# Kernel tuning notes

Measured on AMD Instinct MI355X. Metric: run time of the kernel, lower is better.

## Reference

```python
import jax, jax.numpy as jnp
import numpy as np
import math

N = 50000          # nodes
E = 1000000        # edges (avg degree 20)
NGRAPH = 64        # graphs in batch
CIN = 16           # input scalar channels (16x0e)
C = 32             # hidden multiplicity (mul)
OUT = 100          # output scalars per graph (100x0e)
NB = 10            # number_of_basis
MAX_RADIUS = 3.5
NUM_NEIGH = 20.0
NUM_NODES = 781.25 # 50000 / 64


def setup_inputs() -> dict:
    key = jax.random.key(0)
    ks = jax.random.split(key, 24)
    def p(k, shape, fan):
        return jax.random.normal(k, shape, jnp.float32) / math.sqrt(fan)
    inp = {}
    inp['pos'] = jax.random.normal(ks[0], (N, 3), jnp.float32)
    inp['x'] = jax.random.normal(ks[1], (N, CIN), jnp.float32)
    inp['z'] = jnp.ones((N, 1), jnp.float32)
    inp['edge_index'] = jax.random.randint(ks[2], (2, E), 0, N)
    inp['edge_shift'] = jnp.zeros((E, 3), jnp.float32)
    inp['lattice'] = jax.random.normal(ks[3], (NGRAPH, 3, 3), jnp.float32) * 0.01
    inp['batch'] = jnp.sort(jax.random.randint(ks[4], (N,), 0, NGRAPH))
    inp['fc1_w0'] = p(ks[5], (NB, 100), NB)
    inp['fc1_w1'] = p(ks[6], (100, 2 * CIN), 100)
    inp['sc1'] = p(ks[7], (CIN, 2 * C), CIN)
    inp['lin1_s'] = p(ks[8], (CIN, 2 * C), CIN)
    inp['lin1_v'] = p(ks[9], (CIN, C), CIN)
    inp['fc2_w0'] = p(ks[10], (NB, 100), NB)
    inp['fc2_w1'] = p(ks[11], (100, 5 * C), 100)
    inp['sc2_s'] = p(ks[12], (C, 2 * C), C)
    inp['sc2_v'] = p(ks[13], (C, C), C)
    inp['lin2_s'] = p(ks[14], (C, 2 * C), C)
    inp['lin2_v'] = p(ks[15], (C, C), C)
    inp['fco_w0'] = p(ks[16], (NB, 100), NB)
    inp['fco_w1'] = p(ks[17], (100, 2 * C), 100)
    inp['sco'] = p(ks[18], (C, OUT), C)
    inp['lino_s'] = p(ks[19], (C, OUT), C)
    return inp


def _edge_features(pos, edge_index, edge_shift, lattice, batch):
    src, dst = edge_index[0], edge_index[1]
    ebatch = batch[src]
    # preprocess: edge vectors with periodic shift correction
    edge_vec = pos[dst] - pos[src] + jnp.einsum('ni,nij->nj', edge_shift, lattice[ebatch])
    r = jnp.linalg.norm(edge_vec, axis=1)
    rhat = edge_vec / jnp.maximum(r, 1e-12)[:, None]
    # spherical harmonics lmax=1, component normalization: Y0 = 1, Y1 = sqrt(3) * rhat
    sh0 = jnp.ones_like(r)
    sh1 = math.sqrt(3.0) * rhat
    # soft_one_hot_linspace, basis='gaussian', cutoff=False, scaled by sqrt(NB)
    values = jnp.linspace(0.0, MAX_RADIUS, NB)
    step = values[1] - values[0]
    diff = (r[:, None] - values[None, :]) / step
    basis = jnp.exp(-diff * diff) / 1.12 * math.sqrt(NB)
    # smooth_cutoff(r / max_radius)
    u = 2.0 * (r / MAX_RADIUS - 1.0)
    cut = jnp.where(u > 0, 0.0, jnp.where(u < -2.0, 1.0, 0.5 * (1.0 - jnp.cos(math.pi * u))))
    return src, dst, cut * sh0, cut[:, None] * sh1, basis


def _seg(m, dst):
    return jax.ops.segment_sum(m, dst, num_segments=N) / math.sqrt(NUM_NEIGH)


def reference(pos, x, z, edge_index, edge_shift, lattice, batch,
              fc1_w0, fc1_w1, sc1, lin1_s, lin1_v,
              fc2_w0, fc2_w1, sc2_s, sc2_v, lin2_s, lin2_v,
              fco_w0, fco_w1, sco, lino_s):
    src, dst, sh0, sh1, basis = _edge_features(pos, edge_index, edge_shift, lattice, batch)

    # ---- layer 1: 16x0e input -> gated (C x 0e, C x 1o) ----
    w = jax.nn.silu(basis @ fc1_w0) @ fc1_w1           # (E, 2*CIN) radial weights
    s_src = x[src]                                     # (E, CIN)
    m_s = w[:, :CIN] * s_src * sh0[:, None]            # 0e x Y0 -> 0e
    m_v = (w[:, CIN:] * s_src)[:, :, None] * sh1[:, None, :]  # 0e x Y1 -> 1o
    a_s = _seg(m_s, dst)                               # (N, CIN)
    a_v = _seg(m_v, dst)                               # (N, CIN, 3)
    s_h = (x * z) @ sc1 + a_s @ lin1_s                 # (N, 2C) scalars+gates
    v_h = jnp.einsum('nci,co->noi', a_v, lin1_v)       # (N, C, 3)
    s = jax.nn.silu(s_h[:, :C])
    v = v_h * jax.nn.sigmoid(s_h[:, C:])[:, :, None]

    # ---- layer 2: (C x 0e, C x 1o) -> gated (C x 0e, C x 1o) ----
    w = jax.nn.silu(basis @ fc2_w0) @ fc2_w1           # (E, 5C)
    w1, w2, w3, w4, w5 = jnp.split(w, 5, axis=1)
    ss = s[src]                                        # (E, C)
    vs = v[src]                                        # (E, C, 3)
    m_s = w1 * ss * sh0[:, None] + w2 * jnp.einsum('eci,ei->ec', vs, sh1)
    m_v = (w3 * ss)[:, :, None] * sh1[:, None, :] \
        + w4[:, :, None] * vs * sh0[:, None, None] \
        + w5[:, :, None] * jnp.cross(vs, sh1[:, None, :])
    a_s = _seg(m_s, dst)
    a_v = _seg(m_v, dst)
    s_h = (s * z) @ sc2_s + a_s @ lin2_s
    v_h = jnp.einsum('nci,co->noi', v, sc2_v) + jnp.einsum('nci,co->noi', a_v, lin2_v)
    s2 = jax.nn.silu(s_h[:, :C])
    v2 = v_h * jax.nn.sigmoid(s_h[:, C:])[:, :, None]

    # ---- output convolution: -> 100x0e per node ----
    w = jax.nn.silu(basis @ fco_w0) @ fco_w1           # (E, 2C)
    w1, w2 = jnp.split(w, 2, axis=1)
    m = w1 * s2[src] * sh0[:, None] + w2 * jnp.einsum('eci,ei->ec', v2[src], sh1)
    a = _seg(m, dst)                                   # (N, C)
    out_nodes = (s2 * z) @ sco + a @ lino_s            # (N, OUT)

    # reduce_output: scatter over graphs, divide sqrt(num_nodes)
    out = jax.ops.segment_sum(out_nodes, batch, num_segments=NGRAPH) / math.sqrt(NUM_NODES)
    return out
```

## Files before the change

kernel.cpp:

```cpp
#include <hip/hip_runtime.h>
#include <hip/hip_bf16.h>

#define NN 50000
#define EE 1000000
#define NGRAPHS 64
#define NB_N 196
#define NB_E 3907
#define NB_X 3125
#define NTAB 4096
#define SPL 16

#define INV_SQRT_NEIGH 0.22360679774997896f
#define INV_SQRT_NODES 0.035777087639996634f
#define SQRT3 1.7320508075688772f
#define BSCALE 2.8234621879136734f
#define BSTEP 0.3888888888888889f
#define INV_BSTEP 2.5714285714285716f
#define PI_F 3.14159265358979323846f
#define TAB_DR (3.5f / 4095.0f)
#define TAB_SCALE (4095.0f / 3.5f)

__device__ __forceinline__ float silu_f(float x) { return x / (1.0f + __expf(-x)); }
__device__ __forceinline__ float sigm_f(float x) { return 1.0f / (1.0f + __expf(-x)); }

__device__ __forceinline__ unsigned short f2bf(float f) {
    union { float f; unsigned u; } v; v.f = f;
    unsigned r = v.u + 0x7fffu + ((v.u >> 16) & 1u);
    return (unsigned short)(r >> 16);
}
__device__ __forceinline__ unsigned pk2(float a, float b) {
    return (unsigned)f2bf(a) | ((unsigned)f2bf(b) << 16);
}
__device__ __forceinline__ float bflo(unsigned u) { return __uint_as_float(u << 16); }
__device__ __forceinline__ float bfhi(unsigned u) { return __uint_as_float(u & 0xffff0000u); }

__global__ __launch_bounds__(256) void k_tab(
    const float* __restrict__ fc1w0, const float* __restrict__ fc1w1,
    const float* __restrict__ fc2w0, const float* __restrict__ fc2w1,
    const float* __restrict__ fcow0, const float* __restrict__ fcow1,
    float* __restrict__ tab1, unsigned short* __restrict__ tab2b,
    unsigned short* __restrict__ tab3b)
{
    __shared__ float h[3][100];
    int entry = blockIdx.x;
    int t = threadIdx.x;
    float r = entry * TAB_DR;
    float b[10];
#pragma unroll
    for (int i = 0; i < 10; ++i) {
        float d = (r - (float)i * BSTEP) * INV_BSTEP;
        b[i] = __expf(-d * d) * BSCALE;
    }
    for (int job = t; job < 300; job += 256) {
        int tb = job / 100;
        int j = job - tb * 100;
        const float* w0 = (tb == 0) ? fc1w0 : (tb == 1 ? fc2w0 : fcow0);
        float a = 0.0f;
#pragma unroll
        for (int i = 0; i < 10; ++i) a += b[i] * w0[i * 100 + j];
        h[tb][j] = silu_f(a);
    }
    __syncthreads();
    if (t < 32) {
        float acc = 0.0f;
        for (int j = 0; j < 100; ++j) acc += h[0][j] * fc1w1[j * 32 + t];
        tab1[(size_t)entry * 32 + t] = acc;
    } else if (t < 192) {
        int o = t - 32;
        float acc = 0.0f;
        for (int j = 0; j < 100; ++j) acc += h[1][j] * fc2w1[j * 160 + o];
        tab2b[((size_t)entry * 32 + (o & 31)) * 8 + (o >> 5)] = f2bf(acc);
    } else {
        int o = t - 192;
        float acc = 0.0f;
        for (int j = 0; j < 100; ++j) acc += h[2][j] * fcow1[j * 64 + o];
        tab3b[((size_t)entry * 32 + (o & 31)) * 2 + (o >> 5)] = f2bf(acc);
    }
}

__global__ __launch_bounds__(256) void k_pre2(
    const int* __restrict__ batch, int* __restrict__ gstart,
    const int* __restrict__ ei, int* __restrict__ deg,
    const float* __restrict__ x, unsigned short* __restrict__ row0)
{
    int blk = blockIdx.x;
    if (blk < NB_N) {
        int n = blk * 256 + threadIdx.x;
        if (n >= NN) return;
        int b = batch[n];
        if (n == 0) { for (int g = 0; g <= b; ++g) gstart[g] = 0; }
        else {
            int pb = batch[n - 1];
            for (int g = pb + 1; g <= b; ++g) gstart[g] = n;
        }
        if (n == NN - 1) { for (int g = b + 1; g <= NGRAPHS; ++g) gstart[g] = NN; }
    } else if (blk < NB_N + NB_E) {
        int e = (blk - NB_N) * 256 + threadIdx.x;
        if (e < EE) atomicAdd(&deg[ei[EE + e]], 1);
    } else {
        int idx = (blk - NB_N - NB_E) * 256 + threadIdx.x;
        if (idx < NN * 16) row0[idx] = f2bf(x[idx]);
    }
}

__global__ __launch_bounds__(256) void k_scan1(const int* __restrict__ deg, int* __restrict__ bsum)
{
    __shared__ int sd[256];
    int t = threadIdx.x;
    int i = blockIdx.x * 256 + t;
    sd[t] = (i < NN) ? deg[i] : 0;
    __syncthreads();
#pragma unroll
    for (int o = 128; o > 0; o >>= 1) {
        if (t < o) sd[t] += sd[t + o];
        __syncthreads();
    }
    if (t == 0) bsum[blockIdx.x] = sd[0];
}

__global__ void k_scan2(const int* __restrict__ bsum, int* __restrict__ boff, int* __restrict__ rowp)
{
    if (threadIdx.x == 0) {
        int acc = 0;
        for (int b = 0; b < NB_N; ++b) { boff[b] = acc; acc += bsum[b]; }
        rowp[NN] = EE;
    }
}

__global__ __launch_bounds__(256) void k_scan3(
    const int* __restrict__ deg, const int* __restrict__ boff,
    int* __restrict__ rowp, int* __restrict__ cursor)
{
    __shared__ int sd[256];
    int t = threadIdx.x;
    int i = blockIdx.x * 256 + t;
    int v = (i < NN) ? deg[i] : 0;
    sd[t] = v;
    __syncthreads();
#pragma unroll
    for (int o = 1; o < 256; o <<= 1) {
        int xv = 0;
        if (t >= o) xv = sd[t - o];
        __syncthreads();
        sd[t] += xv;
        __syncthreads();
    }
    if (i < NN) {
        int val = boff[blockIdx.x] + sd[t] - v;
        rowp[i] = val;
        cursor[i] = val;
    }
}

__global__ __launch_bounds__(256) void k_geom(
    const float* __restrict__ pos, const int* __restrict__ ei,
    const float* __restrict__ eshift, const float* __restrict__ lat,
    const int* __restrict__ batch, int* __restrict__ cursor,
    uint4* __restrict__ rec)
{
    int e = blockIdx.x * 256 + threadIdx.x;
    if (e >= EE) return;
    int src = ei[e];
    int dst = ei[EE + e];
    int g = batch[src];
    const float* L = lat + g * 9;
    float t0 = eshift[e*3+0], t1 = eshift[e*3+1], t2 = eshift[e*3+2];
    float vx = pos[dst*3+0] - pos[src*3+0] + t0*L[0] + t1*L[3] + t2*L[6];
    float vy = pos[dst*3+1] - pos[src*3+1] + t0*L[1] + t1*L[4] + t2*L[7];
    float vz = pos[dst*3+2] - pos[src*3+2] + t0*L[2] + t1*L[5] + t2*L[8];
    float r = sqrtf(vx*vx + vy*vy + vz*vz);
    float u = 2.0f * (r * (1.0f/3.5f) - 1.0f);
    float cut;
    if (u > 0.0f) cut = 0.0f;
    else if (u < -2.0f) cut = 1.0f;
    else cut = 0.5f * (1.0f - __cosf(PI_F * u));
    float inv = 1.0f / fmaxf(r, 1e-12f);
    float sc = SQRT3 * cut * inv;
    int i0 = (int)fminf(r * TAB_SCALE + 0.5f, 4095.0f);
    int slot = atomicAdd(&cursor[dst], 1);
    rec[slot] = make_uint4(pk2(sc * vx, sc * vy), pk2(sc * vz, 0.0f),
                           (unsigned)src | ((unsigned)i0 << 17),
                           __float_as_uint(cut));
}

#define EREC_DECODE(E)                                  \
    float cs_ = __uint_as_float((E).w);                 \
    float cx_ = bflo((E).x);                            \
    float cy_ = bfhi((E).x);                            \
    float cz_ = bflo((E).y);                            \
    int src_ = (int)((E).z & 0x1ffffu);                 \
    int i0_ = (int)((E).z >> 17);

#define F1_EDGE(E, ACC) {                                           \
    EREC_DECODE(E)                                                  \
    float w_ = tab1[(size_t)i0_ * 32 + toff];                       \
    float xs_ = __uint_as_float((unsigned)row0[src_ * 16 + c] << 16); \
    float gs_ = (q == 0) ? cs_ : (q == 1 ? cx_ : (q == 2 ? cy_ : cz_)); \
    ACC += w_ * xs_ * gs_; }

__global__ __launch_bounds__(256) void k_fuse1(
    const int* __restrict__ rowp, const uint4* __restrict__ rec,
    const float* __restrict__ tab1, const unsigned short* __restrict__ row0,
    float* __restrict__ a1)
{
    int wid = (blockIdx.x * 256 + threadIdx.x) >> 6;
    int l = threadIdx.x & 63;
    if (wid >= NN) return;
    int b0 = __builtin_amdgcn_readfirstlane(rowp[wid]);
    int b1 = __builtin_amdgcn_readfirstlane(rowp[wid + 1]);
    int q = l >> 4, c = l & 15;
    int toff = (q ? 16 : 0) + c;
    float aA = 0.0f, aB = 0.0f, aC = 0.0f, aD = 0.0f;
    int s = b0;
    for (; s + 3 < b1; s += 4) {
        uint4 eA = rec[s], eB = rec[s+1], eC = rec[s+2], eD = rec[s+3];
        F1_EDGE(eA, aA) F1_EDGE(eB, aB) F1_EDGE(eC, aC) F1_EDGE(eD, aD)
    }
    for (; s < b1; ++s) {
        uint4 eA = rec[s];
        F1_EDGE(eA, aA)
    }
    a1[(size_t)wid * 64 + l] = (aA + aB) + (aC + aD);
}

#define F2_EDGE(E, AS, AX, AY, AZ) {                                \
    EREC_DECODE(E)                                                  \
    uint4 tv_ = ((const uint4*)tab2b)[(size_t)i0_ * 32 + c];        \
    uint2 rv_ = ((const uint2*)row1)[(size_t)src_ * 32 + c];        \
    float w1_ = bflo(tv_.x), w2_ = bfhi(tv_.x);                     \
    float w3_ = bflo(tv_.y), w4_ = bfhi(tv_.y);                     \
    float w5_ = bflo(tv_.z);                                        \
    float sv_ = bflo(rv_.x), vx_ = bfhi(rv_.x);                     \
    float vy_ = bflo(rv_.y), vz_ = bfhi(rv_.y);                     \
    float dot_ = vx_ * cx_ + vy_ * cy_ + vz_ * cz_;                 \
    float w3s_ = w3_ * sv_, w4c_ = w4_ * cs_;                       \
    AS += w1_ * sv_ * cs_ + w2_ * dot_;                             \
    AX += w3s_ * cx_ + w4c_ * vx_ + w5_ * (vy_ * cz_ - vz_ * cy_);  \
    AY += w3s_ * cy_ + w4c_ * vy_ + w5_ * (vz_ * cx_ - vx_ * cz_);  \
    AZ += w3s_ * cz_ + w4c_ * vz_ + w5_ * (vx_ * cy_ - vy_ * cx_); }

__global__ __launch_bounds__(256) void k_fuse2(
    const int* __restrict__ rowp, const uint4* __restrict__ rec,
    const unsigned short* __restrict__ tab2b, const unsigned short* __restrict__ row1,
    float* __restrict__ a2)
{
    int wid = (blockIdx.x * 256 + threadIdx.x) >> 6;
    int l = threadIdx.x & 63;
    if (wid >= NN) return;
    int b0 = __builtin_amdgcn_readfirstlane(rowp[wid]);
    int b1 = __builtin_amdgcn_readfirstlane(rowp[wid + 1]);
    int p = l >> 5, c = l & 31;
    float s0 = 0, x0 = 0, y0 = 0, z0 = 0;
    float s1a = 0, x1 = 0, y1 = 0, z1 = 0;
    int s = b0 + p;
    for (; s + 4 < b1; s += 6) {
        uint4 eA = rec[s], eB = rec[s+2], eC = rec[s+4];
        F2_EDGE(eA, s0, x0, y0, z0)
        F2_EDGE(eB, s1a, x1, y1, z1)
        F2_EDGE(eC, s0, x0, y0, z0)
    }
    for (; s < b1; s += 2) {
        uint4 eA = rec[s];
        F2_EDGE(eA, s1a, x1, y1, z1)
    }
    float mS = s0 + s1a, mX = x0 + x1, mY = y0 + y1, mZ = z0 + z1;
    mS += __shfl_xor(mS, 32);
    mX += __shfl_xor(mX, 32);
    mY += __shfl_xor(mY, 32);
    mZ += __shfl_xor(mZ, 32);
    if (p == 0) {
        float* ap = a2 + (size_t)wid * 128;
        ap[c]      = mS;
        ap[32 + c] = mX;
        ap[64 + c] = mY;
        ap[96 + c] = mZ;
    }
}

#define F3_EDGE(E, ACC) {                                           \
    EREC_DECODE(E)                                                  \
    unsigned tv_ = ((const unsigned*)tab3b)[(size_t)i0_ * 32 + c];  \
    uint2 rv_ = ((const uint2*)row2)[(size_t)src_ * 32 + c];        \
    float w1_ = bflo(tv_), w2_ = bfhi(tv_);                         \
    float sv_ = bflo(rv_.x), vx_ = bfhi(rv_.x);                     \
    float vy_ = bflo(rv_.y), vz_ = bfhi(rv_.y);                     \
    float dot_ = vx_ * cx_ + vy_ * cy_ + vz_ * cz_;                 \
    ACC += w1_ * sv_ * cs_ + w2_ * dot_; }

__global__ __launch_bounds__(256) void k_fuse3(
    const int* __restrict__ rowp, const uint4* __restrict__ rec,
    const unsigned short* __restrict__ tab3b, const unsigned short* __restrict__ row2,
    float* __restrict__ a3)
{
    int wid = (blockIdx.x * 256 + threadIdx.x) >> 6;
    int l = threadIdx.x & 63;
    if (wid >= NN) return;
    int b0 = __builtin_amdgcn_readfirstlane(rowp[wid]);
    int b1 = __builtin_amdgcn_readfirstlane(rowp[wid + 1]);
    int p = l >> 5, c = l & 31;
    float aA = 0.0f, aB = 0.0f;
    int s = b0 + p;
    for (; s + 6 < b1; s += 8) {
        uint4 eA = rec[s], eB = rec[s+2], eC = rec[s+4], eD = rec[s+6];
        F3_EDGE(eA, aA) F3_EDGE(eB, aB) F3_EDGE(eC, aA) F3_EDGE(eD, aB)
    }
    for (; s < b1; s += 2) {
        uint4 eA = rec[s];
        F3_EDGE(eA, aA)
    }
    float acc = aA + aB;
    acc += __shfl_xor(acc, 32);
    if (p == 0) a3[(size_t)wid * 32 + c] = acc;
}

__global__ __launch_bounds__(256) void k_node1(
    const float* __restrict__ x, const float* __restrict__ z,
    const float* __restrict__ a1,
    const float* __restrict__ sc1, const float* __restrict__ lin1s,
    const float* __restrict__ lin1v,
    float* __restrict__ s1, float* __restrict__ v1,
    ushort4* __restrict__ row1)
{
    int n = blockIdx.x * 256 + threadIdx.x;
    if (n >= NN) return;
    float zz = z[n];
    float xs[16], as[16];
#pragma unroll
    for (int c = 0; c < 16; ++c) {
        xs[c] = x[n * 16 + c] * zz;
        as[c] = a1[n * 64 + c] * INV_SQRT_NEIGH;
    }
    float sh[64];
#pragma unroll
    for (int o = 0; o < 64; ++o) sh[o] = 0.0f;
    for (int c = 0; c < 16; ++c) {
        float xc = xs[c], ac = as[c];
#pragma unroll
        for (int o = 0; o < 64; ++o)
            sh[o] += xc * sc1[c * 64 + o] + ac * lin1s[c * 64 + o];
    }
    float sout[32], gate[32];
#pragma unroll
    for (int o = 0; o < 32; ++o) {
        sout[o] = silu_f(sh[o]);
        s1[n * 32 + o] = sout[o];
        gate[o] = sigm_f(sh[32 + o]);
    }
    float vout[3][32];
#pragma unroll
    for (int i = 0; i < 3; ++i) {
        float av[16];
#pragma unroll
        for (int c = 0; c < 16; ++c) av[c] = a1[n * 64 + 16 + i * 16 + c] * INV_SQRT_NEIGH;
        float vh[32];
#pragma unroll
        for (int o = 0; o < 32; ++o) vh[o] = 0.0f;
        for (int c = 0; c < 16; ++c) {
            float ac = av[c];
#pragma unroll
            for (int o = 0; o < 32; ++o) vh[o] += ac * lin1v[c * 32 + o];
        }
#pragma unroll
        for (int o = 0; o < 32; ++o) {
            float v = vh[o] * gate[o];
            v1[(n * 3 + i) * 32 + o] = v;
            vout[i][o] = v;
        }
    }
    ushort4* rp = row1 + (size_t)n * 32;
#pragma unroll
    for (int o = 0; o < 32; ++o)
        rp[o] = make_ushort4(f2bf(sout[o]), f2bf(vout[0][o]), f2bf(vout[1][o]), f2bf(vout[2][o]));
}

__global__ __launch_bounds__(256) void k_node2(
    const float* __restrict__ z,
    const float* __restrict__ s1, const float* __restrict__ v1,
    const float* __restrict__ a2,
    const float* __restrict__ sc2s, const float* __restrict__ sc2v,
    const float* __restrict__ lin2s, const float* __restrict__ lin2v,
    float* __restrict__ s2, ushort4* __restrict__ row2)
{
    int n = blockIdx.x * 256 + threadIdx.x;
    if (n >= NN) return;
    float zz = z[n];
    float sv[32], as[32];
#pragma unroll
    for (int c = 0; c < 32; ++c) {
        sv[c] = s1[n * 32 + c] * zz;
        as[c] = a2[(size_t)n * 128 + c] * INV_SQRT_NEIGH;
    }
    float sh[64];
#pragma unroll
    for (int o = 0; o < 64; ++o) sh[o] = 0.0f;
    for (int c = 0; c < 32; ++c) {
        float a = sv[c], d = as[c];
#pragma unroll
        for (int o = 0; o < 64; ++o)
            sh[o] += a * sc2s[c * 64 + o] + d * lin2s[c * 64 + o];
    }
    float sout[32], gate[32];
#pragma unroll
    for (int o = 0; o < 32; ++o) {
        sout[o] = silu_f(sh[o]);
        s2[n * 32 + o] = sout[o];
        gate[o] = sigm_f(sh[32 + o]);
    }
    float vout[3][32];
#pragma unroll
    for (int i = 0; i < 3; ++i) {
        float vv[32], av[32];
#pragma unroll
        for (int c = 0; c < 32; ++c) {
            vv[c] = v1[(n * 3 + i) * 32 + c];
            av[c] = a2[(size_t)n * 128 + 32 + i * 32 + c] * INV_SQRT_NEIGH;
        }
        float vh[32];
#pragma unroll
        for (int o = 0; o < 32; ++o) vh[o] = 0.0f;
        for (int c = 0; c < 32; ++c) {
            float a = vv[c], d = av[c];
#pragma unroll
            for (int o = 0; o < 32; ++o)
                vh[o] += a * sc2v[c * 32 + o] + d * lin2v[c * 32 + o];
        }
#pragma unroll
        for (int o = 0; o < 32; ++o) vout[i][o] = vh[o] * gate[o];
    }
    ushort4* rp = row2 + (size_t)n * 32;
#pragma unroll
    for (int o = 0; o < 32; ++o)
        rp[o] = make_ushort4(f2bf(sout[o]), f2bf(vout[0][o]), f2bf(vout[1][o]), f2bf(vout[2][o]));
}

__global__ __launch_bounds__(256) void k_red(
    const float* __restrict__ z, const int* __restrict__ gstart,
    const float* __restrict__ s2, const float* __restrict__ a3,
    float* __restrict__ pbuf)
{
    int g  = blockIdx.x >> 4;
    int sp = blockIdx.x & (SPL - 1);
    int n0 = gstart[g], n1 = gstart[g + 1];
    int per = (n1 - n0 + SPL - 1) / SPL;
    int a = n0 + sp * per;
    int b = a + per; if (b > n1) b = n1;
    int t = threadIdx.x;
    int comp = t & 63;
    int lane = t >> 6;
    float acc = 0.0f;
    for (int n = a + lane; n < b; n += 4) {
        if (comp < 32) acc += s2[n * 32 + comp] * z[n];
        else           acc += a3[(size_t)n * 32 + (comp - 32)];
    }
    __shared__ float sd[256];
    sd[t] = acc;
    __syncthreads();
    if (t < 64)
        pbuf[(size_t)blockIdx.x * 64 + t] = sd[t] + sd[t + 64] + sd[t + 128] + sd[t + 192];
}

__global__ __launch_bounds__(128) void k_out2(
    const float* __restrict__ pbuf, const float* __restrict__ sco,
    const float* __restrict__ lino, float* __restrict__ out)
{
    __shared__ float A[32], B[32];
    int g = blockIdx.x;
    int t = threadIdx.x;
    if (t < 64) {
        float v = 0.0f;
        for (int sp = 0; sp < SPL; ++sp)
            v += pbuf[(size_t)(g * SPL + sp) * 64 + t];
        if (t < 32) A[t] = v;
        else        B[t - 32] = v * INV_SQRT_NEIGH;
    }
    __syncthreads();
    if (t < 100) {
        float res = 0.0f;
#pragma unroll
        for (int c = 0; c < 32; ++c)
            res += A[c] * sco[c * 100 + t] + B[c] * lino[c * 100 + t];
        out[g * 100 + t] = res * INV_SQRT_NODES;
    }
}

extern "C" void kernel_launch(void* const* d_in, const int* in_sizes, int n_in,
                              void* d_out, int out_size, void* d_ws, size_t ws_size,
                              hipStream_t stream)
{
    const float* pos   = (const float*)d_in[0];
    const float* x     = (const float*)d_in[1];
    const float* z     = (const float*)d_in[2];
    const int*   ei    = (const int*)d_in[3];
    const float* esh   = (const float*)d_in[4];
    const float* lat   = (const float*)d_in[5];
    const int*   batch = (const int*)d_in[6];
    const float* fc1w0 = (const float*)d_in[7];
    const float* fc1w1 = (const float*)d_in[8];
    const float* sc1   = (const float*)d_in[9];
    const float* lin1s = (const float*)d_in[10];
    const float* lin1v = (const float*)d_in[11];
    const float* fc2w0 = (const float*)d_in[12];
    const float* fc2w1 = (const float*)d_in[13];
    const float* sc2s  = (const float*)d_in[14];
    const float* sc2v  = (const float*)d_in[15];
    const float* lin2s = (const float*)d_in[16];
    const float* lin2v = (const float*)d_in[17];
    const float* fcow0 = (const float*)d_in[18];
    const float* fcow1 = (const float*)d_in[19];
    const float* sco   = (const float*)d_in[20];
    const float* lino  = (const float*)d_in[21];
    float* out = (float*)d_out;

    char* cur = (char*)d_ws;
    auto alloc = [&](size_t bytes) { char* r = cur; cur += (bytes + 15) & ~(size_t)15; return r; };

    float* a1    = (float*)alloc((size_t)NN * 64 * 4);
    float* a2    = (float*)alloc((size_t)NN * 128 * 4);
    float* a3    = (float*)alloc((size_t)NN * 32 * 4);
    float* s1    = (float*)alloc((size_t)NN * 32 * 4);
    float* v1    = (float*)alloc((size_t)NN * 96 * 4);
    float* s2    = (float*)alloc((size_t)NN * 32 * 4);
    unsigned short* row0 = (unsigned short*)alloc((size_t)NN * 16 * 2);
    ushort4* row1 = (ushort4*)alloc((size_t)NN * 32 * 8);
    ushort4* row2 = (ushort4*)alloc((size_t)NN * 32 * 8);
    float* tab1  = (float*)alloc((size_t)NTAB * 32 * 4);
    unsigned short* tab2b = (unsigned short*)alloc((size_t)NTAB * 32 * 8 * 2);
    unsigned short* tab3b = (unsigned short*)alloc((size_t)NTAB * 32 * 2 * 2);
    float* pbuf  = (float*)alloc((size_t)NGRAPHS * SPL * 64 * 4);
    int* deg     = (int*)alloc((size_t)NN * 4);
    int* rowp    = (int*)alloc((size_t)(NN + 4) * 4);
    int* cursor  = (int*)alloc((size_t)NN * 4);
    int* bsum    = (int*)alloc(256 * 4);
    int* boff    = (int*)alloc(256 * 4);
    int* gstart  = (int*)alloc(68 * 4);
    uint4* rec   = (uint4*)alloc((size_t)EE * 16);

    (void)hipMemsetAsync(deg, 0, (size_t)NN * 4, stream);

    k_tab<<<NTAB, 256, 0, stream>>>(fc1w0, fc1w1, fc2w0, fc2w1, fcow0, fcow1,
                                    tab1, tab2b, tab3b);
    k_pre2<<<NB_N + NB_E + NB_X, 256, 0, stream>>>(batch, gstart, ei, deg, x, row0);

    k_scan1<<<NB_N, 256, 0, stream>>>(deg, bsum);
    k_scan2<<<1, 64, 0, stream>>>(bsum, boff, rowp);
    k_scan3<<<NB_N, 256, 0, stream>>>(deg, boff, rowp, cursor);
    k_geom <<<NB_E, 256, 0, stream>>>(pos, ei, esh, lat, batch, cursor, rec);

    int fb = (NN * 64 + 255) / 256;
    k_fuse1<<<fb, 256, 0, stream>>>(rowp, rec, tab1, row0, a1);
    k_node1<<<NB_N, 256, 0, stream>>>(x, z, a1, sc1, lin1s, lin1v, s1, v1, row1);
    k_fuse2<<<fb, 256, 0, stream>>>(rowp, rec, tab2b, (const unsigned short*)row1, a2);
    k_node2<<<NB_N, 256, 0, stream>>>(z, s1, v1, a2, sc2s, sc2v, lin2s, lin2v, s2, row2);
    k_fuse3<<<fb, 256, 0, stream>>>(rowp, rec, tab3b, (const unsigned short*)row2, a3);
    k_red<<<NGRAPHS * SPL, 256, 0, stream>>>(z, gstart, s2, a3, pbuf);
    k_out2<<<NGRAPHS, 128, 0, stream>>>(pbuf, sco, lino, out);
}
```

Baseline: 419.2 us.

## Map node update kernels to one wavefront per node with lane-parallel outputs

k_node1 and k_node2 now assign a 64-lane wavefront to each node instead of one thread per node. Each lane computes one output channel and gets input channels by wave shuffles, and the vector part splits the reduction across two half-waves combined with shfl_xor. This removes the large per-thread register arrays, which likely caused spills and low occupancy, and replaces strided per-thread loads with coalesced ones. In exchange there are many more threads, more shuffles, and some lanes sitting idle during stores.

New measurement: 409.3 us. 1.02x faster.

```diff
diff --git a/kernel.cpp b/kernel.cpp
--- a/kernel.cpp
+++ b/kernel.cpp
@@ -321,56 +321,41 @@
     float* __restrict__ s1, float* __restrict__ v1,
     ushort4* __restrict__ row1)
 {
-    int n = blockIdx.x * 256 + threadIdx.x;
-    if (n >= NN) return;
-    float zz = z[n];
-    float xs[16], as[16];
+    int wid = (blockIdx.x * 256 + threadIdx.x) >> 6;
+    int l = threadIdx.x & 63;
+    if (wid >= NN) return;
+    float zz = z[wid];
+    float a1v = a1[(size_t)wid * 64 + l] * INV_SQRT_NEIGH;
+    float xv = (l < 16) ? x[wid * 16 + l] * zz : 0.0f;
+    float sh = 0.0f;
 #pragma unroll
     for (int c = 0; c < 16; ++c) {
-        xs[c] = x[n * 16 + c] * zz;
-        as[c] = a1[n * 64 + c] * INV_SQRT_NEIGH;
-    }
-    float sh[64];
-#pragma unroll
-    for (int o = 0; o < 64; ++o) sh[o] = 0.0f;
-    for (int c = 0; c < 16; ++c) {
-        float xc = xs[c], ac = as[c];
-#pragma unroll
-        for (int o = 0; o < 64; ++o)
-            sh[o] += xc * sc1[c * 64 + o] + ac * lin1s[c * 64 + o];
-    }
-    float sout[32], gate[32];
-#pragma unroll
-    for (int o = 0; o < 32; ++o) {
-        sout[o] = silu_f(sh[o]);
-        s1[n * 32 + o] = sout[o];
-        gate[o] = sigm_f(sh[32 + o]);
-    }
-    float vout[3][32];
+        float xc = __shfl(xv, c);
+        float ac = __shfl(a1v, c);
+        sh += xc * sc1[c * 64 + l] + ac * lin1s[c * 64 + l];
+    }
+    float sout = silu_f(sh);
+    float gv = sigm_f(sh);
+    int o = l & 31, p = l >> 5;
+    if (l < 32) s1[wid * 32 + l] = sout;
+    float gate_o = __shfl(gv, 32 + o);
+    float vres[3];
 #pragma unroll
     for (int i = 0; i < 3; ++i) {
-        float av[16];
-#pragma unroll
-        for (int c = 0; c < 16; ++c) av[c] = a1[n * 64 + 16 + i * 16 + c] * INV_SQRT_NEIGH;
-        float vh[32];
-#pragma unroll
-        for (int o = 0; o < 32; ++o) vh[o] = 0.0f;
-        for (int c = 0; c < 16; ++c) {
-            float ac = av[c];
-#pragma unroll
-            for (int o = 0; o < 32; ++o) vh[o] += ac * lin1v[c * 32 + o];
+        float acc = 0.0f;
+#pragma unroll
+        for (int k = 0; k < 8; ++k) {
+            int c = p * 8 + k;
+            float ac = __shfl(a1v, 16 + i * 16 + c);
+            acc += ac * lin1v[c * 32 + o];
         }
-#pragma unroll
-        for (int o = 0; o < 32; ++o) {
-            float v = vh[o] * gate[o];
-            v1[(n * 3 + i) * 32 + o] = v;
-            vout[i][o] = v;
-        }
-    }
-    ushort4* rp = row1 + (size_t)n * 32;
-#pragma unroll
-    for (int o = 0; o < 32; ++o)
-        rp[o] = make_ushort4(f2bf(sout[o]), f2bf(vout[0][o]), f2bf(vout[1][o]), f2bf(vout[2][o]));
+        acc += __shfl_xor(acc, 32);
+        vres[i] = acc * gate_o;
+        if (p == 0) v1[(wid * 3 + i) * 32 + o] = vres[i];
+    }
+    if (p == 0)
+        row1[(size_t)wid * 32 + o] =
+            make_ushort4(f2bf(sout), f2bf(vres[0]), f2bf(vres[1]), f2bf(vres[2]));
 }
 
 __global__ __launch_bounds__(256) void k_node2(
@@ -381,56 +366,44 @@
     const float* __restrict__ lin2s, const float* __restrict__ lin2v,
     float* __restrict__ s2, ushort4* __restrict__ row2)
 {
-    int n = blockIdx.x * 256 + threadIdx.x;
-    if (n >= NN) return;
-    float zz = z[n];
-    float sv[32], as[32];
+    int wid = (blockIdx.x * 256 + threadIdx.x) >> 6;
+    int l = threadIdx.x & 63;
+    if (wid >= NN) return;
+    float zz = z[wid];
+    float aLo = a2[(size_t)wid * 128 + l] * INV_SQRT_NEIGH;
+    float aHi = a2[(size_t)wid * 128 + 64 + l] * INV_SQRT_NEIGH;
+    float s1v = (l < 32) ? s1[wid * 32 + l] * zz : 0.0f;
+    float vLo = v1[(size_t)wid * 96 + l];
+    float vHi = (l < 32) ? v1[(size_t)wid * 96 + 64 + l] : 0.0f;
+    float sh = 0.0f;
 #pragma unroll
     for (int c = 0; c < 32; ++c) {
-        sv[c] = s1[n * 32 + c] * zz;
-        as[c] = a2[(size_t)n * 128 + c] * INV_SQRT_NEIGH;
-    }
-    float sh[64];
-#pragma unroll
-    for (int o = 0; o < 64; ++o) sh[o] = 0.0f;
-    for (int c = 0; c < 32; ++c) {
-        float a = sv[c], d = as[c];
-#pragma unroll
-        for (int o = 0; o < 64; ++o)
-            sh[o] += a * sc2s[c * 64 + o] + d * lin2s[c * 64 + o];
-    }
-    float sout[32], gate[32];
-#pragma unroll
-    for (int o = 0; o < 32; ++o) {
-        sout[o] = silu_f(sh[o]);
-        s2[n * 32 + o] = sout[o];
-        gate[o] = sigm_f(sh[32 + o]);
-    }
-    float vout[3][32];
+        float sv = __shfl(s1v, c);
+        float ac = __shfl(aLo, c);
+        sh += sv * sc2s[c * 64 + l] + ac * lin2s[c * 64 + l];
+    }
+    float sout = silu_f(sh);
+    float gv = sigm_f(sh);
+    int o = l & 31, p = l >> 5;
+    if (l < 32) s2[wid * 32 + l] = sout;
+    float gate_o = __shfl(gv, 32 + o);
+    float vres[3];
 #pragma unroll
     for (int i = 0; i < 3; ++i) {
-        float vv[32], av[32];
-#pragma unroll
-        for (int c = 0; c < 32; ++c) {
-            vv[c] = v1[(n * 3 + i) * 32 + c];
-            av[c] = a2[(size_t)n * 128 + 32 + i * 32 + c] * INV_SQRT_NEIGH;
+        float acc = 0.0f;
+#pragma unroll
+        for (int k = 0; k < 16; ++k) {
+            int c = p * 16 + k;
+            float vv = (i == 0) ? __shfl(vLo, c) : (i == 1) ? __shfl(vLo, 32 + c) : __shfl(vHi, c);
+            float av = (i == 0) ? __shfl(aLo, 32 + c) : (i == 1) ? __shfl(aHi, c) : __shfl(aHi, 32 + c);
+            acc += vv * sc2v[c * 32 + o] + av * lin2v[c * 32 + o];
         }
-        float vh[32];
-#pragma unroll
-        for (int o = 0; o < 32; ++o) vh[o] = 0.0f;
-        for (int c = 0; c < 32; ++c) {
-            float a = vv[c], d = av[c];
-#pragma unroll
-            for (int o = 0; o < 32; ++o)
-                vh[o] += a * sc2v[c * 32 + o] + d * lin2v[c * 32 + o];
-        }
-#pragma unroll
-        for (int o = 0; o < 32; ++o) vout[i][o] = vh[o] * gate[o];
-    }
-    ushort4* rp = row2 + (size_t)n * 32;
-#pragma unroll
-    for (int o = 0; o < 32; ++o)
-        rp[o] = make_ushort4(f2bf(sout[o]), f2bf(vout[0][o]), f2bf(vout[1][o]), f2bf(vout[2][o]));
+        acc += __shfl_xor(acc, 32);
+        vres[i] = acc * gate_o;
+    }
+    if (p == 0)
+        row2[(size_t)wid * 32 + o] =
+            make_ushort4(f2bf(sout), f2bf(vres[0]), f2bf(vres[1]), f2bf(vres[2]));
 }
 
 __global__ __launch_bounds__(256) void k_red(
@@ -548,9 +521,9 @@
 
     int fb = (NN * 64 + 255) / 256;
     k_fuse1<<<fb, 256, 0, stream>>>(rowp, rec, tab1, row0, a1);
-    k_node1<<<NB_N, 256, 0, stream>>>(x, z, a1, sc1, lin1s, lin1v, s1, v1, row1);
+    k_node1<<<fb, 256, 0, stream>>>(x, z, a1, sc1, lin1s, lin1v, s1, v1, row1);
     k_fuse2<<<fb, 256, 0, stream>>>(rowp, rec, tab2b, (const unsigned short*)row1, a2);
-    k_node2<<<NB_N, 256, 0, stream>>>(z, s1, v1, a2, sc2s, sc2v, lin2s, lin2v, s2, row2);
+    k_node2<<<fb, 256, 0, stream>>>(z, s1, v1, a2, sc2s, sc2v, lin2s, lin2v, s2, row2);
     k_fuse3<<<fb, 256, 0, stream>>>(rowp, rec, tab3b, (const unsigned short*)row2, a3);
     k_red<<<NGRAPHS * SPL, 256, 0, stream>>>(z, gstart, s2, a3, pbuf);
     k_out2<<<NGRAPHS, 128, 0, stream>>>(pbuf, sco, lino, out);
```

## Tile node update kernels: 32 nodes per block, 8 threads per node via LDS

Applied to the files above, without the earlier changes.

k_node1 and k_node2 previously used one thread per node, with large per-thread register arrays and strided global loads across only 196 blocks. They now stage 32 nodes' inputs into shared memory with coalesced float4 loads, and split each node's output channels across 8 threads with float4 weight reads. The launch grows to 1563 blocks to improve occupancy, coalescing and register pressure. In exchange it adds two block-wide barriers per kernel and uses more shared memory per block.

Measured after the change: 398.6 us. 1.05x faster.

```diff
diff --git a/kernel.cpp b/kernel.cpp
--- a/kernel.cpp
+++ b/kernel.cpp
@@ -7,6 +7,7 @@
 #define NB_N 196
 #define NB_E 3907
 #define NB_X 3125
+#define NB_T 1563
 #define NTAB 4096
 #define SPL 16
 
@@ -321,56 +322,80 @@
     float* __restrict__ s1, float* __restrict__ v1,
     ushort4* __restrict__ row1)
 {
-    int n = blockIdx.x * 256 + threadIdx.x;
-    if (n >= NN) return;
-    float zz = z[n];
-    float xs[16], as[16];
+    __shared__ float xz[32][20];
+    __shared__ float am[32][68];
+    __shared__ float shb[32][68];
+    int t = threadIdx.x;
+    int base = blockIdx.x * 32;
+    if (t < 128) {
+        int node = t >> 2, rem = t & 3;
+        if (base + node < NN)
+            *(float4*)&xz[node][rem * 4] = ((const float4*)x)[(size_t)(base + node) * 4 + rem];
+    }
+#pragma unroll
+    for (int k = 0; k < 2; ++k) {
+        int f = k * 256 + t;
+        int node = f >> 4, rem = f & 15;
+        if (base + node < NN)
+            *(float4*)&am[node][rem * 4] = ((const float4*)a1)[(size_t)(base + node) * 16 + rem];
+    }
+    __syncthreads();
+    int node = t >> 3, og = t & 7;
+    int gnode = base + node;
+    float zz = (gnode < NN) ? z[gnode] : 0.0f;
+    int o0 = og * 8;
+    float acc[8];
+#pragma unroll
+    for (int k = 0; k < 8; ++k) acc[k] = 0.0f;
 #pragma unroll
     for (int c = 0; c < 16; ++c) {
-        xs[c] = x[n * 16 + c] * zz;
-        as[c] = a1[n * 64 + c] * INV_SQRT_NEIGH;
-    }
-    float sh[64];
-#pragma unroll
-    for (int o = 0; o < 64; ++o) sh[o] = 0.0f;
-    for (int c = 0; c < 16; ++c) {
-        float xc = xs[c], ac = as[c];
-#pragma unroll
-        for (int o = 0; o < 64; ++o)
-            sh[o] += xc * sc1[c * 64 + o] + ac * lin1s[c * 64 + o];
-    }
-    float sout[32], gate[32];
-#pragma unroll
-    for (int o = 0; o < 32; ++o) {
-        sout[o] = silu_f(sh[o]);
-        s1[n * 32 + o] = sout[o];
-        gate[o] = sigm_f(sh[32 + o]);
-    }
-    float vout[3][32];
+        float xc = xz[node][c] * zz;
+        float ac = am[node][c] * INV_SQRT_NEIGH;
+        float4 wa = *(const float4*)&sc1[c * 64 + o0];
+        float4 wb = *(const float4*)&sc1[c * 64 + o0 + 4];
+        float4 la = *(const float4*)&lin1s[c * 64 + o0];
+        float4 lb = *(const float4*)&lin1s[c * 64 + o0 + 4];
+        acc[0] += xc * wa.x + ac * la.x;
+        acc[1] += xc * wa.y + ac * la.y;
+        acc[2] += xc * wa.z + ac * la.z;
+        acc[3] += xc * wa.w + ac * la.w;
+        acc[4] += xc * wb.x + ac * lb.x;
+        acc[5] += xc * wb.y + ac * lb.y;
+        acc[6] += xc * wb.z + ac * lb.z;
+        acc[7] += xc * wb.w + ac * lb.w;
+    }
+#pragma unroll
+    for (int k = 0; k < 8; ++k) shb[node][o0 + k] = acc[k];
+    __syncthreads();
+    int o0v = og * 4;
+    float vres[3][4];
 #pragma unroll
     for (int i = 0; i < 3; ++i) {
-        float av[16];
-#pragma unroll
-        for (int c = 0; c < 16; ++c) av[c] = a1[n * 64 + 16 + i * 16 + c] * INV_SQRT_NEIGH;
-        float vh[32];
-#pragma unroll
-        for (int o = 0; o < 32; ++o) vh[o] = 0.0f;
+        float a4[4] = {0.0f, 0.0f, 0.0f, 0.0f};
+#pragma unroll
         for (int c = 0; c < 16; ++c) {
-            float ac = av[c];
-#pragma unroll
-            for (int o = 0; o < 32; ++o) vh[o] += ac * lin1v[c * 32 + o];
+            float av = am[node][16 + i * 16 + c] * INV_SQRT_NEIGH;
+            float4 lv = *(const float4*)&lin1v[c * 32 + o0v];
+            a4[0] += av * lv.x; a4[1] += av * lv.y;
+            a4[2] += av * lv.z; a4[3] += av * lv.w;
         }
 #pragma unroll
-        for (int o = 0; o < 32; ++o) {
-            float v = vh[o] * gate[o];
-            v1[(n * 3 + i) * 32 + o] = v;
-            vout[i][o] = v;
+        for (int k = 0; k < 4; ++k) vres[i][k] = a4[k];
+    }
+    if (gnode < NN) {
+#pragma unroll
+        for (int k = 0; k < 4; ++k) {
+            float so = silu_f(shb[node][o0v + k]);
+            float gt = sigm_f(shb[node][32 + o0v + k]);
+            float v0 = vres[0][k] * gt, v1v = vres[1][k] * gt, v2v = vres[2][k] * gt;
+            s1[gnode * 32 + o0v + k] = so;
+            v1[(gnode * 3 + 0) * 32 + o0v + k] = v0;
+            v1[(gnode * 3 + 1) * 32 + o0v + k] = v1v;
+            v1[(gnode * 3 + 2) * 32 + o0v + k] = v2v;
+            row1[(size_t)gnode * 32 + o0v + k] =
+                make_ushort4(f2bf(so), f2bf(v0), f2bf(v1v), f2bf(v2v));
         }
     }
-    ushort4* rp = row1 + (size_t)n * 32;
-#pragma unroll
-    for (int o = 0; o < 32; ++o)
-        rp[o] = make_ushort4(f2bf(sout[o]), f2bf(vout[0][o]), f2bf(vout[1][o]), f2bf(vout[2][o]));
 }
 
 __global__ __launch_bounds__(256) void k_node2(
@@ -381,56 +406,89 @@
     const float* __restrict__ lin2s, const float* __restrict__ lin2v,
     float* __restrict__ s2, ushort4* __restrict__ row2)
 {
-    int n = blockIdx.x * 256 + threadIdx.x;
-    if (n >= NN) return;
-    float zz = z[n];
-    float sv[32], as[32];
-#pragma unroll
+    __shared__ float s1s[32][36];
+    __shared__ float vv[32][100];
+    __shared__ float am[32][132];
+    __shared__ float shb[32][68];
+    int t = threadIdx.x;
+    int base = blockIdx.x * 32;
+    {
+        int node = t >> 3, rem = t & 7;
+        if (base + node < NN)
+            *(float4*)&s1s[node][rem * 4] = ((const float4*)s1)[(size_t)(base + node) * 8 + rem];
+    }
+#pragma unroll
+    for (int k = 0; k < 3; ++k) {
+        int f = k * 256 + t;
+        int node = f / 24, rem = f - node * 24;
+        if (base + node < NN)
+            *(float4*)&vv[node][rem * 4] = ((const float4*)v1)[(size_t)(base + node) * 24 + rem];
+    }
+#pragma unroll
+    for (int k = 0; k < 4; ++k) {
+        int f = k * 256 + t;
+        int node = f >> 5, rem = f & 31;
+        if (base + node < NN)
+            *(float4*)&am[node][rem * 4] = ((const float4*)a2)[(size_t)(base + node) * 32 + rem];
+    }
+    __syncthreads();
+    int node = t >> 3, og = t & 7;
+    int gnode = base + node;
+    float zz = (gnode < NN) ? z[gnode] : 0.0f;
+    int o0 = og * 8;
+    float acc[8];
+#pragma unroll
+    for (int k = 0; k < 8; ++k) acc[k] = 0.0f;
+#pragma unroll 8
     for (int c = 0; c < 32; ++c) {
-        sv[c] = s1[n * 32 + c] * zz;
-        as[c] = a2[(size_t)n * 128 + c] * INV_SQRT_NEIGH;
-    }
-    float sh[64];
-#pragma unroll
-    for (int o = 0; o < 64; ++o) sh[o] = 0.0f;
-    for (int c = 0; c < 32; ++c) {
-        float a = sv[c], d = as[c];
-#pragma unroll
-        for (int o = 0; o < 64; ++o)
-            sh[o] += a * sc2s[c * 64 + o] + d * lin2s[c * 64 + o];
-    }
-    float sout[32], gate[32];
-#pragma unroll
-    for (int o = 0; o < 32; ++o) {
-        sout[o] = silu_f(sh[o]);
-        s2[n * 32 + o] = sout[o];
-        gate[o] = sigm_f(sh[32 + o]);
-    }
-    float vout[3][32];
+        float sv = s1s[node][c] * zz;
+        float ac = am[node][c] * INV_SQRT_NEIGH;
+        float4 wa = *(const float4*)&sc2s[c * 64 + o0];
+        float4 wb = *(const float4*)&sc2s[c * 64 + o0 + 4];
+        float4 la = *(const float4*)&lin2s[c * 64 + o0];
+        float4 lb = *(const float4*)&lin2s[c * 64 + o0 + 4];
+        acc[0] += sv * wa.x + ac * la.x;
+        acc[1] += sv * wa.y + ac * la.y;
+        acc[2] += sv * wa.z + ac * la.z;
+        acc[3] += sv * wa.w + ac * la.w;
+        acc[4] += sv * wb.x + ac * lb.x;
+        acc[5] += sv * wb.y + ac * lb.y;
+        acc[6] += sv * wb.z + ac * lb.z;
+        acc[7] += sv * wb.w + ac * lb.w;
+    }
+#pragma unroll
+    for (int k = 0; k < 8; ++k) shb[node][o0 + k] = acc[k];
+    __syncthreads();
+    int o0v = og * 4;
+    float vres[3][4];
 #pragma unroll
     for (int i = 0; i < 3; ++i) {
-        float vv[32], av[32];
-#pragma unroll
+        float a4[4] = {0.0f, 0.0f, 0.0f, 0.0f};
+#pragma unroll 8
         for (int c = 0; c < 32; ++c) {
-            vv[c] = v1[(n * 3 + i) * 32 + c];
-            av[c] = a2[(size_t)n * 128 + 32 + i * 32 + c] * INV_SQRT_NEIGH;
+            float vvv = vv[node][i * 32 + c];
+            float av = am[node][32 + i * 32 + c] * INV_SQRT_NEIGH;
+            float4 wv = *(const float4*)&sc2v[c * 32 + o0v];
+            float4 lv = *(const float4*)&lin2v[c * 32 + o0v];
+            a4[0] += vvv * wv.x + av * lv.x;
+            a4[1] += vvv * wv.y + av * lv.y;
+            a4[2] += vvv * wv.z + av * lv.z;
+            a4[3] += vvv * wv.w + av * lv.w;
         }
-        float vh[32];
-#pragma unroll
-        for (int o = 0; o < 32; ++o) vh[o] = 0.0f;
-        for (int c = 0; c < 32; ++c) {
-            float a = vv[c], d = av[c];
-#pragma unroll
-            for (int o = 0; o < 32; ++o)
-                vh[o] += a * sc2v[c * 32 + o] + d * lin2v[c * 32 + o];
+#pragma unroll
+        for (int k = 0; k < 4; ++k) vres[i][k] = a4[k];
+    }
+    if (gnode < NN) {
+#pragma unroll
+        for (int k = 0; k < 4; ++k) {
+            float so = silu_f(shb[node][o0v + k]);
+            float gt = sigm_f(shb[node][32 + o0v + k]);
+            float v0 = vres[0][k] * gt, v1v = vres[1][k] * gt, v2v = vres[2][k] * gt;
+            s2[gnode * 32 + o0v + k] = so;
+            row2[(size_t)gnode * 32 + o0v + k] =
+                make_ushort4(f2bf(so), f2bf(v0), f2bf(v1v), f2bf(v2v));
         }
-#pragma unroll
-        for (int o = 0; o < 32; ++o) vout[i][o] = vh[o] * gate[o];
-    }
-    ushort4* rp = row2 + (size_t)n * 32;
-#pragma unroll
-    for (int o = 0; o < 32; ++o)
-        rp[o] = make_ushort4(f2bf(sout[o]), f2bf(vout[0][o]), f2bf(vout[1][o]), f2bf(vout[2][o]));
+    }
 }
 
 __global__ __launch_bounds__(256) void k_red(
@@ -548,9 +606,9 @@
 
     int fb = (NN * 64 + 255) / 256;
     k_fuse1<<<fb, 256, 0, stream>>>(rowp, rec, tab1, row0, a1);
-    k_node1<<<NB_N, 256, 0, stream>>>(x, z, a1, sc1, lin1s, lin1v, s1, v1, row1);
+    k_node1<<<NB_T, 256, 0, stream>>>(x, z, a1, sc1, lin1s, lin1v, s1, v1, row1);
     k_fuse2<<<fb, 256, 0, stream>>>(rowp, rec, tab2b, (const unsigned short*)row1, a2);
-    k_node2<<<NB_N, 256, 0, stream>>>(z, s1, v1, a2, sc2s, sc2v, lin2s, lin2v, s2, row2);
+    k_node2<<<NB_T, 256, 0, stream>>>(z, s1, v1, a2, sc2s, sc2v, lin2s, lin2v, s2, row2);
     k_fuse3<<<fb, 256, 0, stream>>>(rowp, rec, tab3b, (const unsigned short*)row2, a3);
     k_red<<<NGRAPHS * SPL, 256, 0, stream>>>(z, gstart, s2, a3, pbuf);
     k_out2<<<NGRAPHS, 128, 0, stream>>>(pbuf, sco, lino, out);
```
